# Kernel tuning notes

Measured on AMD Instinct MI355X. Metric: run time of the kernel, lower is better.

The kernel has to match this reference:

```python
import jax, jax.numpy as jnp
import numpy as np

EMB = 1024
HEAD = 128

def setup_inputs() -> dict:
    key = jax.random.key(0)
    kx, kk, kq, kv = jax.random.split(key, 4)
    s = 1.0 / np.sqrt(EMB)
    return {
        "x": jax.random.normal(kx, (8, 2048, EMB), dtype=jnp.float32),
        "Wk": jax.random.normal(kk, (EMB, HEAD), dtype=jnp.float32) * s,
        "Wq": jax.random.normal(kq, (EMB, HEAD), dtype=jnp.float32) * s,
        "Wv": jax.random.normal(kv, (EMB, HEAD), dtype=jnp.float32) * s,
    }

def reference(x, Wk, Wq, Wv):
    # x: [B,T,E]; projections (no bias)
    k = jnp.einsum('bte,eh->bth', x, Wk)
    q = jnp.einsum('bte,eh->bth', x, Wq)
    v = jnp.einsum('bte,eh->bth', x, Wv)
    # scores: [B,T,T], NOTE: no 1/sqrt(d) scaling in original module
    qk = jnp.einsum('bih,bjh->bij', q, k)
    T = x.shape[1]
    causal = jnp.tril(jnp.ones((T, T), dtype=bool))  # True = keep
    qk = jnp.where(causal, qk, -jnp.inf)
    # NOTE: softmax over axis -2 (query axis), as in original
    attn = jax.nn.softmax(qk, axis=-2)
    return jnp.einsum('bij,bjh->bih', attn, v)
```

## Files before the change

kernel.cpp:

```cpp
#include <hip/hip_runtime.h>

typedef unsigned short u16;
typedef unsigned int u32;
typedef _Float16 f16;
typedef __attribute__((ext_vector_type(8))) _Float16 f16x8;
typedef __attribute__((ext_vector_type(4))) float f32x4;

constexpr int SEQ = 2048;
constexpr int EMBD = 1024;
constexpr int HD = 128;
constexpr int NB = 8;
constexpr int NSLS = 8;
constexpr int NSLP = 4;

__device__ inline u16 f2h(float f) { return __builtin_bit_cast(u16, (f16)f); }
__device__ inline u32 pack2(float a, float b) { return (u32)f2h(a) | ((u32)f2h(b) << 16); }

__device__ inline f32x4 mfma16(f16x8 a, f16x8 b, f32x4 c) {
  return __builtin_amdgcn_mfma_f32_16x16x32_f16(a, b, c, 0, 0, 0);
}

__device__ __forceinline__ void gload16(const u16* g, u16* l) {
  __builtin_amdgcn_global_load_lds(
      (const __attribute__((address_space(1))) u32*)g,
      (__attribute__((address_space(3))) u32*)l, 16, 0, 0);
}

template<int RB>
__device__ inline f16x8 frag_ld(const u16* lds, int row, int e) {
  int byte = row * RB + ((e * 2) ^ ((row & 7) << 4));
  return *reinterpret_cast<const f16x8*>(reinterpret_cast<const char*>(lds) + byte);
}

__global__ __launch_bounds__(256) void k_cvt_w(const float* __restrict__ Wq,
                                               const float* __restrict__ Wk,
                                               const float* __restrict__ Wv,
                                               u16* __restrict__ Wt) {
  int t = blockIdx.x * 256 + threadIdx.x;
  int e0 = (t & 255) * 4;
  int H = t >> 8;
  int w = H >> 7, h = H & 127;
  const float* W = (w == 0) ? Wq : (w == 1) ? Wk : Wv;
  ushort4 o;
  o.x = f2h(W[(size_t)(e0 + 0) * HD + h]);
  o.y = f2h(W[(size_t)(e0 + 1) * HD + h]);
  o.z = f2h(W[(size_t)(e0 + 2) * HD + h]);
  o.w = f2h(W[(size_t)(e0 + 3) * HD + h]);
  int k0t = e0 >> 6, ec = e0 & 63;
  size_t el = (size_t)(k0t * 384 + H) * 64 + (ec ^ ((H & 7) << 3));
  *reinterpret_cast<ushort4*>(Wt + el) = o;
}

__global__ __launch_bounds__(512, 4) void k_proj(const float* __restrict__ x,
                                                 const u16* __restrict__ Wt,
                                                 u16* __restrict__ Qb,
                                                 u16* __restrict__ Kb,
                                                 u16* __restrict__ Vtb) {
  __shared__ __align__(16) u16 As[2][64 * 64];
  __shared__ __align__(16) u16 Bs[2][192 * 64];
  const int mt = blockIdx.x, ny = blockIdx.y;
  const int t = threadIdx.x, lane = t & 63, wave = t >> 6;
  const int rh = (wave & 1) * 32, cq = (wave >> 1) * 48;
  const int ar = t >> 3, ac = t & 7;
  const float* asrc = x + (size_t)(mt * 64 + ar) * EMBD + ac * 8;
  const int adst = ar * 64 + ((ac * 8) ^ ((ar & 7) << 3));
  f32x4 zero = {0.f, 0.f, 0.f, 0.f};
  f32x4 acc[2][3];
#pragma unroll
  for (int a = 0; a < 2; ++a)
#pragma unroll
    for (int b = 0; b < 3; ++b) acc[a][b] = zero;

  float4 xe0, xe1, xo0, xo1;
  xe0 = *reinterpret_cast<const float4*>(asrc);
  xe1 = *reinterpret_cast<const float4*>(asrc + 4);
#pragma unroll
  for (int q = 0; q < 3; ++q) {
    int lin = q * 512 + t;
    gload16(Wt + ny * 12288 + lin * 8, &Bs[0][lin * 8]);
  }
  {
    uint4 o = {pack2(xe0.x, xe0.y), pack2(xe0.z, xe0.w), pack2(xe1.x, xe1.y), pack2(xe1.z, xe1.w)};
    *reinterpret_cast<uint4*>(&As[0][adst]) = o;
  }
  xo0 = *reinterpret_cast<const float4*>(asrc + 64);
  xo1 = *reinterpret_cast<const float4*>(asrc + 68);
  __syncthreads();
#pragma unroll 2
  for (int s = 0; s < 16; ++s) {
    const int cur = s & 1;
    if (s + 1 < 16) {
#pragma unroll
      for (int q = 0; q < 3; ++q) {
        int lin = q * 512 + t;
        gload16(Wt + (s + 1) * 24576 + ny * 12288 + lin * 8, &Bs[cur ^ 1][lin * 8]);
      }
    }
    if (s + 2 < 16) {
      if (cur == 0) {
        xe0 = *reinterpret_cast<const float4*>(asrc + (s + 2) * 64);
        xe1 = *reinterpret_cast<const float4*>(asrc + (s + 2) * 64 + 4);
      } else {
        xo0 = *reinterpret_cast<const float4*>(asrc + (s + 2) * 64);
        xo1 = *reinterpret_cast<const float4*>(asrc + (s + 2) * 64 + 4);
      }
    }
    __builtin_amdgcn_s_setprio(1);
#pragma unroll
    for (int kk = 0; kk < 2; ++kk) {
      f16x8 af0 = frag_ld<128>(As[cur], rh + (lane & 15), kk * 32 + (lane >> 4) * 8);
      f16x8 af1 = frag_ld<128>(As[cur], rh + 16 + (lane & 15), kk * 32 + (lane >> 4) * 8);
#pragma unroll
      for (int fc = 0; fc < 3; ++fc) {
        f16x8 bw = frag_ld<128>(Bs[cur], cq + fc * 16 + (lane & 15), kk * 32 + (lane >> 4) * 8);
        acc[0][fc] = mfma16(af0, bw, acc[0][fc]);
        acc[1][fc] = mfma16(af1, bw, acc[1][fc]);
      }
    }
    __builtin_amdgcn_s_setprio(0);
    if (s + 1 < 16) {
      uint4 o;
      if (cur == 0)
        o = {pack2(xo0.x, xo0.y), pack2(xo0.z, xo0.w), pack2(xo1.x, xo1.y), pack2(xo1.z, xo1.w)};
      else
        o = {pack2(xe0.x, xe0.y), pack2(xe0.z, xe0.w), pack2(xe1.x, xe1.y), pack2(xe1.z, xe1.w)};
      *reinterpret_cast<uint4*>(&As[cur ^ 1][adst]) = o;
    }
    __syncthreads();
  }
#pragma unroll
  for (int fi = 0; fi < 2; ++fi)
#pragma unroll
    for (int fc = 0; fc < 3; ++fc) {
      int gcol = ny * 192 + cq + fc * 16 + (lane & 15);
      int w = gcol >> 7, h = gcol & 127;
      int i0 = mt * 64 + rh + fi * 16 + (lane >> 4) * 4;
      if (w < 2) {
        u16* P = w ? Kb : Qb;
#pragma unroll
        for (int r = 0; r < 4; ++r) {
          int i = i0 + r;
          P[(size_t)i * 128 + (h ^ ((i & 7) << 3))] = f2h(acc[fi][fc][r]);
        }
      } else {
        int bb = i0 >> 11, jt = (i0 >> 6) & 31, tl = i0 & 63;
        ushort4 o = {f2h(acc[fi][fc][0]), f2h(acc[fi][fc][1]),
                     f2h(acc[fi][fc][2]), f2h(acc[fi][fc][3])};
        size_t el = ((size_t)(bb * 32 + jt) * 128 + h) * 64 + (tl ^ ((h & 7) << 3));
        *reinterpret_cast<ushort4*>(Vtb + el) = o;
      }
    }
}

__device__ inline void merge_ml(float& m, float& l, float m2, float l2) {
  float mn = fmaxf(m, m2);
  float a = (m > -1e37f) ? l * __expf(m - mn) : 0.f;
  float b = (m2 > -1e37f) ? l2 * __expf(m2 - mn) : 0.f;
  m = mn;
  l = a + b;
}

__global__ __launch_bounds__(256, 2) void k_statsA(const u16* __restrict__ Qb,
                                                   const u16* __restrict__ Kb,
                                                   float* __restrict__ mpart,
                                                   float* __restrict__ lpart) {
  __shared__ __align__(16) u16 Qs[2][128 * 128];
  const int id = blockIdx.x;
  const int bb = id & 7, zp = (id >> 3) & 7, sl = id >> 6;
  const int t = threadIdx.x, lane = t & 63, wave = t >> 6;
  f32x4 zero = {0.f, 0.f, 0.f, 0.f};

  for (int ph = 0; ph < 2; ++ph) {
    const int jb = ph ? 7 - zp : zp;
    __syncthreads();
#pragma unroll
    for (int q = 0; q < 16; ++q) {
      int lin = q * 256 + t;
      gload16(Kb + ((size_t)bb * SEQ + jb * 256) * 128 + lin * 8, &Qs[0][lin * 8]);
    }
    __syncthreads();
    f16x8 af[4][4];
#pragma unroll
    for (int fj = 0; fj < 4; ++fj)
#pragma unroll
      for (int kk = 0; kk < 4; ++kk) {
        int row = wave * 64 + fj * 16 + (lane & 15);
        af[fj][kk] = frag_ld<256>(Qs[row >> 7], row & 127, kk * 32 + (lane >> 4) * 8);
      }
    float m[4][4], l[4][4];
#pragma unroll
    for (int fj = 0; fj < 4; ++fj)
#pragma unroll
      for (int r = 0; r < 4; ++r) {
        m[fj][r] = -INFINITY;
        l[fj][r] = 0.f;
      }
    __syncthreads();
    const int itb = 2 * jb;
    const int it0 = itb + ((sl - itb) & 7);
    int cur = 0;
    if (it0 < 16) {
#pragma unroll
      for (int q = 0; q < 8; ++q) {
        int lin = q * 256 + t;
        gload16(Qb + ((size_t)bb * SEQ + it0 * 128) * 128 + lin * 8, &Qs[0][lin * 8]);
      }
      for (int it = it0; it < 16; it += 8) {
        __syncthreads();
        if (it + 8 < 16) {
#pragma unroll
          for (int q = 0; q < 8; ++q) {
            int lin = q * 256 + t;
            gload16(Qb + ((size_t)bb * SEQ + (it + 8) * 128) * 128 + lin * 8,
                    &Qs[cur ^ 1][lin * 8]);
          }
        }
        const bool diag = (it <= 2 * jb + 1);
#pragma unroll
        for (int h = 0; h < 2; ++h) {
          f32x4 acc[4][4];
#pragma unroll
          for (int a = 0; a < 4; ++a)
#pragma unroll
            for (int b = 0; b < 4; ++b) acc[a][b] = zero;
          __builtin_amdgcn_s_setprio(1);
#pragma unroll
          for (int kk = 0; kk < 4; ++kk)
#pragma unroll
            for (int fi = 0; fi < 4; ++fi) {
              f16x8 bq = frag_ld<256>(Qs[cur], (h * 4 + fi) * 16 + (lane & 15),
                                      kk * 32 + (lane >> 4) * 8);
#pragma unroll
              for (int fj = 0; fj < 4; ++fj)
                acc[fj][fi] = mfma16(af[fj][kk], bq, acc[fj][fi]);
            }
          __builtin_amdgcn_s_setprio(0);
          if (diag) {
#pragma unroll
            for (int fj = 0; fj < 4; ++fj)
#pragma unroll
              for (int r = 0; r < 4; ++r) {
                int jg = jb * 256 + wave * 64 + fj * 16 + (lane >> 4) * 4 + r;
                float v[4];
                float vmax = -INFINITY;
#pragma unroll
                for (int fi = 0; fi < 4; ++fi) {
                  int ig = it * 128 + (h * 4 + fi) * 16 + (lane & 15);
                  v[fi] = (ig >= jg) ? acc[fj][fi][r] : -INFINITY;
                  vmax = fmaxf(vmax, v[fi]);
                }
                if (vmax > -1e37f) {
                  float mn = fmaxf(m[fj][r], vmax);
                  float sc = (m[fj][r] > -1e37f) ? __expf(m[fj][r] - mn) : 0.f;
                  float ss = 0.f;
#pragma unroll
                  for (int fi = 0; fi < 4; ++fi)
                    ss += (v[fi] > -1e37f) ? __expf(v[fi] - mn) : 0.f;
                  l[fj][r] = l[fj][r] * sc + ss;
                  m[fj][r] = mn;
                }
              }
          } else {
#pragma unroll
            for (int fj = 0; fj < 4; ++fj)
#pragma unroll
              for (int r = 0; r < 4; ++r) {
                float vmax = acc[fj][0][r];
#pragma unroll
                for (int fi = 1; fi < 4; ++fi) vmax = fmaxf(vmax, acc[fj][fi][r]);
                float mn = fmaxf(m[fj][r], vmax);
                float sc = __expf(m[fj][r] - mn);
                float ss = 0.f;
#pragma unroll
                for (int fi = 0; fi < 4; ++fi) ss += __expf(acc[fj][fi][r] - mn);
                l[fj][r] = l[fj][r] * sc + ss;
                m[fj][r] = mn;
              }
          }
        }
        cur ^= 1;
      }
    }
#pragma unroll
    for (int fj = 0; fj < 4; ++fj)
#pragma unroll
      for (int r = 0; r < 4; ++r)
        for (int msk = 1; msk <= 8; msk <<= 1) {
          float m2 = __shfl_xor(m[fj][r], msk);
          float l2 = __shfl_xor(l[fj][r], msk);
          merge_ml(m[fj][r], l[fj][r], m2, l2);
        }
    if ((lane & 15) == 0) {
#pragma unroll
      for (int fj = 0; fj < 4; ++fj)
#pragma unroll
        for (int r = 0; r < 4; ++r) {
          int j = jb * 256 + wave * 64 + fj * 16 + (lane >> 4) * 4 + r;
          size_t idx = (size_t)sl * (NB * SEQ) + (size_t)bb * SEQ + j;
          mpart[idx] = m[fj][r];
          lpart[idx] = l[fj][r];
        }
    }
  }
}

__global__ __launch_bounds__(256) void k_stats_reduce(const float* __restrict__ mpart,
                                                      const float* __restrict__ lpart,
                                                      float* __restrict__ Cg) {
  int idx = blockIdx.x * 256 + threadIdx.x;
  float m = -INFINITY;
#pragma unroll
  for (int sl = 0; sl < NSLS; sl++) m = fmaxf(m, mpart[sl * (NB * SEQ) + idx]);
  float l = 0.f;
#pragma unroll
  for (int sl = 0; sl < NSLS; sl++) {
    float ms = mpart[sl * (NB * SEQ) + idx];
    if (ms > -1e37f) l += lpart[sl * (NB * SEQ) + idx] * __expf(ms - m);
  }
  Cg[idx] = m + __logf(l);
}

__global__ __launch_bounds__(256, 2) void k_passB(const u16* __restrict__ Qb,
                                                  const u16* __restrict__ Kb,
                                                  const u16* __restrict__ Vtb,
                                                  const float* __restrict__ Cg,
                                                  u16* __restrict__ opart) {
  __shared__ __align__(16) u16 Ks2[2][64 * 128];
  __shared__ __align__(16) u16 Vs2[2][128 * 64];
  __shared__ __align__(16) u16 Ps[64 * 64];
  const int id = blockIdx.x;
  const int bb = id & 7, zp = (id >> 3) & 15, sl = id >> 7;
  const int t = threadIdx.x, lane = t & 63, wave = t >> 6;
  f32x4 zero = {0.f, 0.f, 0.f, 0.f};

  auto stageKV = [&](int jt, int b) {
#pragma unroll
    for (int q = 0; q < 4; ++q) {
      int lin = q * 256 + t;
      gload16(Kb + ((size_t)bb * SEQ + jt * 64) * 128 + lin * 8, &Ks2[b][lin * 8]);
    }
#pragma unroll
    for (int q = 0; q < 4; ++q) {
      int lin = q * 256 + t;
      gload16(Vtb + ((size_t)bb * 32 + jt) * 8192 + lin * 8, &Vs2[b][lin * 8]);
    }
  };

  for (int ph = 0; ph < 2; ++ph) {
    const int it = ph ? 31 - zp : zp;
    f16x8 qf[4];
#pragma unroll
    for (int kk = 0; kk < 4; ++kk) {
      size_t gi = (size_t)bb * SEQ + it * 64 + wave * 16 + (lane & 15);
      int e0 = kk * 32 + (lane >> 4) * 8;
      qf[kk] = *reinterpret_cast<const f16x8*>(Qb + gi * 128 + (e0 ^ (((int)gi & 7) << 3)));
    }
    f32x4 accO[8];
#pragma unroll
    for (int b = 0; b < 8; ++b) accO[b] = zero;
    __syncthreads();
    if (sl <= it) stageKV(sl, 0);
    int cur = 0;
    for (int jt = sl; jt <= it; jt += NSLP) {
      __syncthreads();
      if (jt + NSLP <= it) stageKV(jt + NSLP, cur ^ 1);
      float cj[4];
#pragma unroll
      for (int fj = 0; fj < 4; ++fj)
        cj[fj] = Cg[bb * SEQ + jt * 64 + fj * 16 + (lane & 15)];
      f32x4 accS[4];
#pragma unroll
      for (int b = 0; b < 4; ++b) accS[b] = zero;
      __builtin_amdgcn_s_setprio(1);
#pragma unroll
      for (int kk = 0; kk < 4; ++kk)
#pragma unroll
        for (int fj = 0; fj < 4; ++fj) {
          f16x8 bk = frag_ld<256>(Ks2[cur], fj * 16 + (lane & 15), kk * 32 + (lane >> 4) * 8);
          accS[fj] = mfma16(qf[kk], bk, accS[fj]);
        }
      __builtin_amdgcn_s_setprio(0);
#pragma unroll
      for (int fj = 0; fj < 4; ++fj) {
        int jloc = fj * 16 + (lane & 15);
        int jg = jt * 64 + jloc;
        float c = cj[fj];
#pragma unroll
        for (int r = 0; r < 4; ++r) {
          int iloc = wave * 16 + (lane >> 4) * 4 + r;
          int ig = it * 64 + iloc;
          float p = __expf(accS[fj][r] - c);
          if (ig < jg) p = 0.f;
          Ps[iloc * 64 + (jloc ^ ((iloc & 7) << 3))] = f2h(p);
        }
      }
      __builtin_amdgcn_s_setprio(1);
#pragma unroll
      for (int ks = 0; ks < 2; ++ks) {
        f16x8 pa = frag_ld<128>(Ps, wave * 16 + (lane & 15), ks * 32 + (lane >> 4) * 8);
#pragma unroll
        for (int fh = 0; fh < 8; ++fh) {
          f16x8 bv = frag_ld<128>(Vs2[cur], fh * 16 + (lane & 15), ks * 32 + (lane >> 4) * 8);
          accO[fh] = mfma16(pa, bv, accO[fh]);
        }
      }
      __builtin_amdgcn_s_setprio(0);
      cur ^= 1;
    }
#pragma unroll
    for (int fh = 0; fh < 8; ++fh)
#pragma unroll
      for (int r = 0; r < 4; ++r) {
        int ig = it * 64 + wave * 16 + (lane >> 4) * 4 + r;
        int h = fh * 16 + (lane & 15);
        opart[(((size_t)sl * NB + bb) * SEQ + ig) * HD + h] = f2h(accO[fh][r]);
      }
  }
}

__global__ __launch_bounds__(256) void k_reduceB(const u16* __restrict__ opart,
                                                 float* __restrict__ out) {
  size_t base = ((size_t)blockIdx.x * 256 + threadIdx.x) * 8;
  const size_t S = (size_t)NB * SEQ * HD;
  float s[8];
#pragma unroll
  for (int j = 0; j < 8; j++) s[j] = 0.f;
#pragma unroll
  for (int sl = 0; sl < NSLP; sl++) {
    f16x8 v = *reinterpret_cast<const f16x8*>(opart + sl * S + base);
#pragma unroll
    for (int j = 0; j < 8; j++) s[j] += (float)v[j];
  }
  float4 o0 = {s[0], s[1], s[2], s[3]};
  float4 o1 = {s[4], s[5], s[6], s[7]};
  *reinterpret_cast<float4*>(out + base) = o0;
  *reinterpret_cast<float4*>(out + base + 4) = o1;
}

extern "C" void kernel_launch(void* const* d_in, const int* in_sizes, int n_in,
                              void* d_out, int out_size, void* d_ws, size_t ws_size,
                              hipStream_t stream) {
  (void)in_sizes; (void)n_in; (void)out_size; (void)ws_size;
  const float* x = (const float*)d_in[0];
  const float* Wk = (const float*)d_in[1];
  const float* Wq = (const float*)d_in[2];
  const float* Wv = (const float*)d_in[3];
  float* out = (float*)d_out;
  char* ws = (char*)d_ws;

  u16* Wt = (u16*)(ws + 0);
  u16* Qb = (u16*)(ws + 786432);
  u16* Kb = (u16*)(ws + 4980736);
  u16* Vtb = (u16*)(ws + 9175040);
  float* mpart = (float*)(ws + 13369344);
  float* lpart = (float*)(ws + 13893632);
  float* Cg = (float*)(ws + 14417920);
  u16* opart = (u16*)(ws + 14548992);

  k_cvt_w<<<384, 256, 0, stream>>>(Wq, Wk, Wv, Wt);
  k_proj<<<dim3(256, 2), 512, 0, stream>>>(x, Wt, Qb, Kb, Vtb);
  k_statsA<<<512, 256, 0, stream>>>(Qb, Kb, mpart, lpart);
  k_stats_reduce<<<64, 256, 0, stream>>>(mpart, lpart, Cg);
  k_passB<<<512, 256, 0, stream>>>(Qb, Kb, Vtb, Cg, opart);
  k_reduceB<<<1024, 256, 0, stream>>>(opart, out);
}
```

Measured before the change: 94.52 us.

## Restructure column-softmax stats pass to hold Q in registers and stream K tiles

The statistics kernel now keeps a 64-row query slice per wave in registers and streams 32-row K tiles through double-buffered LDS, using 32x32x16 MFMA instead of 16x16x32. Partial max/sum values are written per query slice (32 slices) instead of being accumulated across a K block, and the reduce kernel is updated to combine only the valid slices for each key. This removes the in-register online-softmax rescaling across tiles and shrinks LDS use, but writes many more partial results and makes the reduce kernel read up to 32 slices per key. The workspace offsets are moved to fit the larger partial buffers.

```diff
diff --git a/kernel.cpp b/kernel.cpp
--- a/kernel.cpp
+++ b/kernel.cpp
@@ -5,12 +5,13 @@
 typedef _Float16 f16;
 typedef __attribute__((ext_vector_type(8))) _Float16 f16x8;
 typedef __attribute__((ext_vector_type(4))) float f32x4;
+typedef __attribute__((ext_vector_type(16))) float f32x16;
 
 constexpr int SEQ = 2048;
 constexpr int EMBD = 1024;
 constexpr int HD = 128;
 constexpr int NB = 8;
-constexpr int NSLS = 8;
+constexpr int NISL = 32;
 constexpr int NSLP = 4;
 
 __device__ inline u16 f2h(float f) { return __builtin_bit_cast(u16, (f16)f); }
@@ -18,6 +19,9 @@
 
 __device__ inline f32x4 mfma16(f16x8 a, f16x8 b, f32x4 c) {
   return __builtin_amdgcn_mfma_f32_16x16x32_f16(a, b, c, 0, 0, 0);
+}
+__device__ inline f32x16 mfma32(f16x8 a, f16x8 b, f32x16 c) {
+  return __builtin_amdgcn_mfma_f32_32x32x16_f16(a, b, c, 0, 0, 0);
 }
 
 __device__ __forceinline__ void gload16(const u16* g, u16* l) {
@@ -164,142 +168,96 @@
                                                    const u16* __restrict__ Kb,
                                                    float* __restrict__ mpart,
                                                    float* __restrict__ lpart) {
-  __shared__ __align__(16) u16 Qs[2][128 * 128];
+  __shared__ __align__(16) u16 Ks[2][32 * 128];
   const int id = blockIdx.x;
-  const int bb = id & 7, zp = (id >> 3) & 7, sl = id >> 6;
+  const int bb = id & 7, z = (id >> 3) & 3, slj = id >> 5;
   const int t = threadIdx.x, lane = t & 63, wave = t >> 6;
-  f32x4 zero = {0.f, 0.f, 0.f, 0.f};
+  const int l31 = lane & 31, lh = lane >> 5;
 
   for (int ph = 0; ph < 2; ++ph) {
-    const int jb = ph ? 7 - zp : zp;
+    const int ib = ph ? 7 - z : z;
+    const int i0 = ib * 256;
+    const int iw = i0 + wave * 64;
+    const int islice = ib * 4 + wave;
+    const int jt0 = slj;
+    const int jtmax = 8 * ib + 7;
     __syncthreads();
-#pragma unroll
-    for (int q = 0; q < 16; ++q) {
-      int lin = q * 256 + t;
-      gload16(Kb + ((size_t)bb * SEQ + jb * 256) * 128 + lin * 8, &Qs[0][lin * 8]);
-    }
-    __syncthreads();
-    f16x8 af[4][4];
-#pragma unroll
-    for (int fj = 0; fj < 4; ++fj)
-#pragma unroll
-      for (int kk = 0; kk < 4; ++kk) {
-        int row = wave * 64 + fj * 16 + (lane & 15);
-        af[fj][kk] = frag_ld<256>(Qs[row >> 7], row & 127, kk * 32 + (lane >> 4) * 8);
-      }
-    float m[4][4], l[4][4];
-#pragma unroll
-    for (int fj = 0; fj < 4; ++fj)
-#pragma unroll
-      for (int r = 0; r < 4; ++r) {
-        m[fj][r] = -INFINITY;
-        l[fj][r] = 0.f;
-      }
-    __syncthreads();
-    const int itb = 2 * jb;
-    const int it0 = itb + ((sl - itb) & 7);
-    int cur = 0;
-    if (it0 < 16) {
-#pragma unroll
-      for (int q = 0; q < 8; ++q) {
-        int lin = q * 256 + t;
-        gload16(Qb + ((size_t)bb * SEQ + it0 * 128) * 128 + lin * 8, &Qs[0][lin * 8]);
-      }
-      for (int it = it0; it < 16; it += 8) {
+    f16x8 qa[2][8];
+#pragma unroll
+    for (int hf = 0; hf < 2; ++hf) {
+      size_t gi = (size_t)bb * SEQ + iw + hf * 32 + l31;
+      const u16* qrow = Qb + gi * 128;
+      int sw = ((int)gi & 7) << 3;
+#pragma unroll
+      for (int ks = 0; ks < 8; ++ks)
+        qa[hf][ks] = *reinterpret_cast<const f16x8*>(qrow + ((ks * 16 + lh * 8) ^ sw));
+    }
+    if (jt0 <= jtmax) {
+#pragma unroll
+      for (int q = 0; q < 2; ++q)
+        gload16(Kb + ((size_t)bb * SEQ + jt0 * 32) * 128 + (q * 256 + t) * 8,
+                &Ks[0][(q * 256 + t) * 8]);
+      int cur = 0;
+      for (int jt = jt0; jt <= jtmax; jt += 16) {
         __syncthreads();
-        if (it + 8 < 16) {
-#pragma unroll
-          for (int q = 0; q < 8; ++q) {
-            int lin = q * 256 + t;
-            gload16(Qb + ((size_t)bb * SEQ + (it + 8) * 128) * 128 + lin * 8,
-                    &Qs[cur ^ 1][lin * 8]);
-          }
-        }
-        const bool diag = (it <= 2 * jb + 1);
-#pragma unroll
-        for (int h = 0; h < 2; ++h) {
-          f32x4 acc[4][4];
-#pragma unroll
-          for (int a = 0; a < 4; ++a)
-#pragma unroll
-            for (int b = 0; b < 4; ++b) acc[a][b] = zero;
-          __builtin_amdgcn_s_setprio(1);
-#pragma unroll
-          for (int kk = 0; kk < 4; ++kk)
-#pragma unroll
-            for (int fi = 0; fi < 4; ++fi) {
-              f16x8 bq = frag_ld<256>(Qs[cur], (h * 4 + fi) * 16 + (lane & 15),
-                                      kk * 32 + (lane >> 4) * 8);
-#pragma unroll
-              for (int fj = 0; fj < 4; ++fj)
-                acc[fj][fi] = mfma16(af[fj][kk], bq, acc[fj][fi]);
+        if (jt + 16 <= jtmax) {
+#pragma unroll
+          for (int q = 0; q < 2; ++q)
+            gload16(Kb + ((size_t)bb * SEQ + (jt + 16) * 32) * 128 + (q * 256 + t) * 8,
+                    &Ks[cur ^ 1][(q * 256 + t) * 8]);
+        }
+        f32x16 accS[2];
+#pragma unroll
+        for (int b = 0; b < 2; ++b)
+#pragma unroll
+          for (int q = 0; q < 16; ++q) accS[b][q] = 0.f;
+        __builtin_amdgcn_s_setprio(1);
+#pragma unroll
+        for (int ks = 0; ks < 8; ++ks) {
+          f16x8 bk = frag_ld<256>(Ks[cur], l31, ks * 16 + lh * 8);
+          accS[0] = mfma32(qa[0][ks], bk, accS[0]);
+          accS[1] = mfma32(qa[1][ks], bk, accS[1]);
+        }
+        __builtin_amdgcn_s_setprio(0);
+        const int jg = jt * 32 + l31;
+        float v[2][16];
+        float vmax = -INFINITY;
+        if (jt * 32 + 31 < iw) {
+#pragma unroll
+          for (int hf = 0; hf < 2; ++hf)
+#pragma unroll
+            for (int q = 0; q < 16; ++q) {
+              v[hf][q] = accS[hf][q];
+              vmax = fmaxf(vmax, v[hf][q]);
             }
-          __builtin_amdgcn_s_setprio(0);
-          if (diag) {
-#pragma unroll
-            for (int fj = 0; fj < 4; ++fj)
-#pragma unroll
-              for (int r = 0; r < 4; ++r) {
-                int jg = jb * 256 + wave * 64 + fj * 16 + (lane >> 4) * 4 + r;
-                float v[4];
-                float vmax = -INFINITY;
-#pragma unroll
-                for (int fi = 0; fi < 4; ++fi) {
-                  int ig = it * 128 + (h * 4 + fi) * 16 + (lane & 15);
-                  v[fi] = (ig >= jg) ? acc[fj][fi][r] : -INFINITY;
-                  vmax = fmaxf(vmax, v[fi]);
-                }
-                if (vmax > -1e37f) {
-                  float mn = fmaxf(m[fj][r], vmax);
-                  float sc = (m[fj][r] > -1e37f) ? __expf(m[fj][r] - mn) : 0.f;
-                  float ss = 0.f;
-#pragma unroll
-                  for (int fi = 0; fi < 4; ++fi)
-                    ss += (v[fi] > -1e37f) ? __expf(v[fi] - mn) : 0.f;
-                  l[fj][r] = l[fj][r] * sc + ss;
-                  m[fj][r] = mn;
-                }
-              }
-          } else {
-#pragma unroll
-            for (int fj = 0; fj < 4; ++fj)
-#pragma unroll
-              for (int r = 0; r < 4; ++r) {
-                float vmax = acc[fj][0][r];
-#pragma unroll
-                for (int fi = 1; fi < 4; ++fi) vmax = fmaxf(vmax, acc[fj][fi][r]);
-                float mn = fmaxf(m[fj][r], vmax);
-                float sc = __expf(m[fj][r] - mn);
-                float ss = 0.f;
-#pragma unroll
-                for (int fi = 0; fi < 4; ++fi) ss += __expf(acc[fj][fi][r] - mn);
-                l[fj][r] = l[fj][r] * sc + ss;
-                m[fj][r] = mn;
-              }
-          }
+        } else {
+#pragma unroll
+          for (int hf = 0; hf < 2; ++hf)
+#pragma unroll
+            for (int q = 0; q < 16; ++q) {
+              int ig = iw + hf * 32 + (q & 3) + 8 * (q >> 2) + 4 * lh;
+              v[hf][q] = (ig >= jg) ? accS[hf][q] : -INFINITY;
+              vmax = fmaxf(vmax, v[hf][q]);
+            }
+        }
+        float m = vmax, l = 0.f;
+        if (vmax > -1e37f) {
+#pragma unroll
+          for (int hf = 0; hf < 2; ++hf)
+#pragma unroll
+            for (int q = 0; q < 16; ++q)
+              l += (v[hf][q] > -1e37f) ? __expf(v[hf][q] - m) : 0.f;
+        }
+        float m2 = __shfl_xor(m, 32);
+        float l2 = __shfl_xor(l, 32);
+        merge_ml(m, l, m2, l2);
+        if (lane < 32) {
+          size_t idx = ((size_t)islice * NB + bb) * SEQ + jg;
+          mpart[idx] = m;
+          lpart[idx] = l;
         }
         cur ^= 1;
       }
-    }
-#pragma unroll
-    for (int fj = 0; fj < 4; ++fj)
-#pragma unroll
-      for (int r = 0; r < 4; ++r)
-        for (int msk = 1; msk <= 8; msk <<= 1) {
-          float m2 = __shfl_xor(m[fj][r], msk);
-          float l2 = __shfl_xor(l[fj][r], msk);
-          merge_ml(m[fj][r], l[fj][r], m2, l2);
-        }
-    if ((lane & 15) == 0) {
-#pragma unroll
-      for (int fj = 0; fj < 4; ++fj)
-#pragma unroll
-        for (int r = 0; r < 4; ++r) {
-          int j = jb * 256 + wave * 64 + fj * 16 + (lane >> 4) * 4 + r;
-          size_t idx = (size_t)sl * (NB * SEQ) + (size_t)bb * SEQ + j;
-          mpart[idx] = m[fj][r];
-          lpart[idx] = l[fj][r];
-        }
     }
   }
 }
@@ -308,14 +266,14 @@
                                                       const float* __restrict__ lpart,
                                                       float* __restrict__ Cg) {
   int idx = blockIdx.x * 256 + threadIdx.x;
+  int j = idx & 2047;
+  int isl0 = (j >> 8) * 4;
   float m = -INFINITY;
-#pragma unroll
-  for (int sl = 0; sl < NSLS; sl++) m = fmaxf(m, mpart[sl * (NB * SEQ) + idx]);
+  for (int s = isl0; s < NISL; ++s) m = fmaxf(m, mpart[(size_t)s * 16384 + idx]);
   float l = 0.f;
-#pragma unroll
-  for (int sl = 0; sl < NSLS; sl++) {
-    float ms = mpart[sl * (NB * SEQ) + idx];
-    if (ms > -1e37f) l += lpart[sl * (NB * SEQ) + idx] * __expf(ms - m);
+  for (int s = isl0; s < NISL; ++s) {
+    float ms = mpart[(size_t)s * 16384 + idx];
+    if (ms > -1e37f) l += lpart[(size_t)s * 16384 + idx] * __expf(ms - m);
   }
   Cg[idx] = m + __logf(l);
 }
@@ -453,9 +411,9 @@
   u16* Kb = (u16*)(ws + 4980736);
   u16* Vtb = (u16*)(ws + 9175040);
   float* mpart = (float*)(ws + 13369344);
-  float* lpart = (float*)(ws + 13893632);
-  float* Cg = (float*)(ws + 14417920);
-  u16* opart = (u16*)(ws + 14548992);
+  float* lpart = (float*)(ws + 15466496);
+  float* Cg = (float*)(ws + 17563648);
+  u16* opart = (u16*)(ws + 17629184);
 
   k_cvt_w<<<384, 256, 0, stream>>>(Wq, Wk, Wv, Wt);
   k_proj<<<dim3(256, 2), 512, 0, stream>>>(x, Wt, Qb, Kb, Vtb);
```

After: 90.21 us. 4.6% less time.
